# Kernel tuning notes

Measured on AMD Instinct MI355X. Metric: run time of the kernel, lower is better.

## Reference

```python
import jax, jax.numpy as jnp
import numpy as np

B = 131072            # number of supervoxel areas (vmapped)
H, W = 8, 16          # mask_new / mask_old shape
DX, DY = 16, 16       # diameter_x, diameter_y -> mask_combined / image shape
DIM_STRIDE = 0
TV = 2                # translation_val


def _grad(x, axis):
    # numpy-style gradient, unit spacing: central diff interior, one-sided edges
    x = jnp.moveaxis(x, axis, 0)
    g = jnp.concatenate([x[1:2] - x[0:1], (x[2:] - x[:-2]) * 0.5, x[-1:] - x[-2:-1]], axis=0)
    return jnp.moveaxis(g, 0, axis)


def get_diamond(diameter):
    r = diameter // 2
    def line(curr, idx):
        return jax.lax.dynamic_update_slice(curr, jnp.ones(diameter, jnp.float32), (jnp.abs(r - idx),))
    a = jax.vmap(line)(jnp.zeros((diameter, 2 * diameter), jnp.float32), jnp.arange(diameter)).astype(bool)
    b = jnp.flip(a)[:, diameter:]   # flip over both axes, keep right half
    a = a[:, :-diameter]
    return jnp.logical_and(a, b).astype(jnp.float32)


def translate(mask, axis, is_forward, tv, shape):
    lo = tv * (1 - is_forward)
    hi = shape[axis] - tv * is_forward
    m = jnp.take(mask, jnp.arange(lo, hi), axis=axis)
    pad = [[0, 0], [0, 0]]
    pad[axis][1 - is_forward] = tv
    return jnp.pad(m, pad)


def features(image, mask):
    mi = image * mask
    s = jnp.sum(mask)
    mean = jnp.sum(mi) / s
    var = jnp.sum(((mi - mean) * mask) ** 2) / s
    return jnp.stack([mean, var])


def single(image, mn, mo, diamond):
    # consistency loss
    p = jnp.pad(mo, ((1, 1), (1, 1)))
    g = _grad(p, DIM_STRIDE) ** 2
    g = g[1:-1, 1:-1]
    consistency = jnp.mean(jnp.maximum(mn - (g * 5.0 + mo * 5.0), 0.0))
    # intertwine 'f h w -> (h f) w'
    mc = jnp.stack([mn, mo], axis=1).reshape(DX, DY)
    rounding = jnp.mean(-((mc - (1.0 - mc)) ** 2))
    feats = jnp.stack([
        features(image, translate(mc, 0, 0, TV, (DX, DY))),
        features(image, translate(mc, 0, 1, TV, (DX, DY))),
        features(image, translate(mc, 1, 0, TV, (DX, DY))),
        features(image, translate(mc, 1, 1, TV, (DX, DY)))])
    fvar = jnp.mean(jnp.var(feats, axis=0))
    gi = _grad(image, DIM_STRIDE)
    gm = _grad(mc, DIM_STRIDE)
    edge = jnp.mean(0.5 * (gi - gm) ** 2 * gi)   # optax.l2_loss scaled by image gradient
    avg_cov = jnp.mean(0.5 * (mc - diamond) ** 2)
    mi = mc * image
    out_image = mc * (jnp.sum(mi) / jnp.sum(mc))
    return mc, out_image, consistency, rounding, fvar, edge, avg_cov


def setup_inputs() -> dict:
    key = jax.random.key(0)
    k1, k2, k3 = jax.random.split(key, 3)
    return {
        "resized_image": jax.random.normal(k1, (B, DX, DY), jnp.float32),
        "mask_new": jax.random.uniform(k2, (B, H, W), jnp.float32),
        "mask_old": jax.random.uniform(k3, (B, H, W), jnp.float32),
    }


def reference(resized_image, mask_new, mask_old):
    diamond = jnp.pad(get_diamond(DX - 1), ((0, 1), (0, 1)))  # (DX, DY)
    return jax.vmap(lambda im, mn, mo: single(im, mn, mo, diamond))(resized_image, mask_new, mask_old)
```

## Files before the change

kernel.cpp:

```cpp
#include <hip/hip_runtime.h>

template<int CTRL>
__device__ __forceinline__ float dppf(float v) {
    return __int_as_float(__builtin_amdgcn_update_dpp(
        0, __float_as_int(v), CTRL, 0xF, 0xF, true));
}

__device__ __forceinline__ float bfly16(float v) {
    v += dppf<0xB1>(v);
    v += dppf<0x4E>(v);
    v += dppf<0x141>(v);
    v += dppf<0x140>(v);
    return v;
}

__global__ __launch_bounds__(256) void apply_area_kernel(
    const float* __restrict__ img_g,
    const float* __restrict__ mn_g,
    const float* __restrict__ mo_g,
    float* __restrict__ out,
    int B)
{
    const int lane = threadIdx.x & 63;
    const int w    = threadIdx.x >> 6;
    const int q    = lane >> 4;
    const int c    = lane & 15;
    const int b    = blockIdx.x * 16 + w * 4 + q;
    if (b >= B) return;

    const float* imp = img_g + (size_t)b * 256 + c;
    const float* mnp = mn_g  + (size_t)b * 128 + c;
    const float* mop = mo_g  + (size_t)b * 128 + c;

    float im[16], mc[16];
#pragma unroll
    for (int r = 0; r < 16; ++r) im[r] = imp[r * 16];
#pragma unroll
    for (int i = 0; i < 8; ++i) {
        mc[2 * i]     = mnp[i * 16];
        mc[2 * i + 1] = mop[i * 16];
    }

    float c_acc = 0.f;
#pragma unroll
    for (int i = 0; i < 8; ++i) {
        float mo_i = mc[2 * i + 1];
        float mo_m = (i > 0) ? mc[2 * i - 1] : 0.f;
        float mo_p = (i < 7) ? mc[2 * i + 3] : 0.f;
        float g = 0.5f * (mo_p - mo_m);
        c_acc += fmaxf(mc[2 * i] - 5.f * (g * g + mo_i), 0.f);
    }

    float e_acc = 0.f, r_acc = 0.f, a_acc = 0.f, smi = 0.f, S1 = 0.f, S2 = 0.f;
#pragma unroll
    for (int r = 0; r < 16; ++r) {
        float gi = (r == 0)  ? im[1] - im[0]
                 : (r == 15) ? im[15] - im[14]
                 : 0.5f * (im[r + 1] - im[r - 1]);
        float gm = (r == 0)  ? mc[1] - mc[0]
                 : (r == 15) ? mc[15] - mc[14]
                 : 0.5f * (mc[r + 1] - mc[r - 1]);
        float d = gi - gm;
        e_acc += 0.5f * d * d * gi;
        float tw = 2.f * mc[r] - 1.f;
        r_acc += tw * tw;
        int abr = (r > 7) ? r - 7 : 7 - r;
        float dia = (r < 15 && c >= abr && c <= 14 - abr) ? 1.f : 0.f;
        float dd = mc[r] - dia;
        a_acc += 0.5f * dd * dd;
        S1 += mc[r];
        S2 += mc[r] * mc[r];
        smi += mc[r] * im[r];
    }

    float B0 = 0, D0 = 0, E0 = 0, B1 = 0, D1 = 0, E1 = 0;
    float B2 = 0, D2 = 0, E2 = 0, B3 = 0, D3 = 0, E3 = 0;
#pragma unroll
    for (int r = 0; r < 16; ++r) {
        float t0v = (r < 14) ? mc[r + 2] : 0.f;
        float t1v = (r >= 2) ? mc[r - 2] : 0.f;
        float t2v = dppf<0x102>(mc[r]);
        float t3v = dppf<0x112>(mc[r]);
#define ACC(t, Bx, Dx, Ex) { float mi_ = (t) * im[r]; float tt_ = (t) * (t); \
        Bx += mi_; Dx = fmaf(tt_, mi_, Dx); float tm_ = (t) * mi_; Ex = fmaf(tm_, tm_, Ex); }
        ACC(t0v, B0, D0, E0)
        ACC(t1v, B1, D1, E1)
        ACC(t2v, B2, D2, E2)
        ACC(t3v, B3, D3, E3)
#undef ACC
    }
    float A0 = S1 - mc[0] - mc[1];
    float C0 = S2 - mc[0] * mc[0] - mc[1] * mc[1];
    float A1 = S1 - mc[14] - mc[15];
    float C1 = S2 - mc[14] * mc[14] - mc[15] * mc[15];
    float A2 = dppf<0x102>(S1), C2 = dppf<0x102>(S2);
    float A3 = dppf<0x112>(S1), C3 = dppf<0x112>(S2);

    c_acc = bfly16(c_acc); r_acc = bfly16(r_acc);
    e_acc = bfly16(e_acc); a_acc = bfly16(a_acc);
    float smc = bfly16(S1); smi = bfly16(smi);
    A0 = bfly16(A0); A1 = bfly16(A1); A2 = bfly16(A2); A3 = bfly16(A3);
    B0 = bfly16(B0); B1 = bfly16(B1); B2 = bfly16(B2); B3 = bfly16(B3);
    C0 = bfly16(C0); C1 = bfly16(C1); C2 = bfly16(C2); C3 = bfly16(C3);
    D0 = bfly16(D0); D1 = bfly16(D1); D2 = bfly16(D2); D3 = bfly16(D3);
    E0 = bfly16(E0); E1 = bfly16(E1); E2 = bfly16(E2); E3 = bfly16(E3);

    const float scale = smi / smc;

    float* mco = out + (size_t)b * 256 + c;
    float* oio = out + (size_t)B * 256 + (size_t)b * 256 + c;
#pragma unroll
    for (int r = 0; r < 16; ++r) {
        mco[r * 16] = mc[r];
        oio[r * 16] = mc[r] * scale;
    }

    if (c == 0) {
        float m0 = B0 / A0, m1 = B1 / A1, m2 = B2 / A2, m3 = B3 / A3;
        float v0 = (E0 - 2.f * m0 * D0 + m0 * m0 * C0) / A0;
        float v1 = (E1 - 2.f * m1 * D1 + m1 * m1 * C1) / A1;
        float v2 = (E2 - 2.f * m2 * D2 + m2 * m2 * C2) / A2;
        float v3 = (E3 - 2.f * m3 * D3 + m3 * m3 * C3) / A3;

        float fm = 0.25f * (m0 + m1 + m2 + m3);
        float dm0 = m0 - fm, dm1 = m1 - fm, dm2 = m2 - fm, dm3 = m3 - fm;
        float vm = 0.25f * (dm0 * dm0 + dm1 * dm1 + dm2 * dm2 + dm3 * dm3);
        float fv = 0.25f * (v0 + v1 + v2 + v3);
        float dv0 = v0 - fv, dv1 = v1 - fv, dv2 = v2 - fv, dv3 = v3 - fv;
        float vv = 0.25f * (dv0 * dv0 + dv1 * dv1 + dv2 * dv2 + dv3 * dv3);

        float* s = out + (size_t)B * 512;
        s[b]                 = c_acc * (1.f / 128.f);
        s[(size_t)B + b]     = -r_acc * (1.f / 256.f);
        s[2 * (size_t)B + b] = 0.5f * (vm + vv);
        s[3 * (size_t)B + b] = e_acc * (1.f / 256.f);
        s[4 * (size_t)B + b] = a_acc * (1.f / 256.f);
    }
}

extern "C" void kernel_launch(void* const* d_in, const int* in_sizes, int n_in,
                              void* d_out, int out_size, void* d_ws, size_t ws_size,
                              hipStream_t stream) {
    const float* img = (const float*)d_in[0];
    const float* mn  = (const float*)d_in[1];
    const float* mo  = (const float*)d_in[2];
    float* out = (float*)d_out;
    const int B = in_sizes[0] / 256;
    const int blocks = (B + 15) / 16;
    apply_area_kernel<<<blocks, 256, 0, stream>>>(img, mn, mo, out, B);
}
```

Before: 105.2 us.

## Process two columns per lane with float2 accesses and nontemporal stores

Remaps each area onto 8 lanes, each handling two adjacent columns, so loads and stores use 64-bit vector accesses and cross-lane reductions shrink to 8-lane butterflies. Neighbor-column shifts now use row-shift-by-one DPP with boundary masks, since two areas share a DPP row. Output stores become nontemporal to avoid polluting caches. This halves thread count per area and raises per-thread register use.

```diff
diff --git a/kernel.cpp b/kernel.cpp
--- a/kernel.cpp
+++ b/kernel.cpp
@@ -1,4 +1,6 @@
 #include <hip/hip_runtime.h>
+
+typedef float vf2 __attribute__((ext_vector_type(2)));
 
 template<int CTRL>
 __device__ __forceinline__ float dppf(float v) {
@@ -6,11 +8,10 @@
         0, __float_as_int(v), CTRL, 0xF, 0xF, true));
 }
 
-__device__ __forceinline__ float bfly16(float v) {
+__device__ __forceinline__ float bfly8(float v) {
     v += dppf<0xB1>(v);
     v += dppf<0x4E>(v);
     v += dppf<0x141>(v);
-    v += dppf<0x140>(v);
     return v;
 }
 
@@ -23,99 +24,106 @@
 {
     const int lane = threadIdx.x & 63;
     const int w    = threadIdx.x >> 6;
-    const int q    = lane >> 4;
-    const int c    = lane & 15;
-    const int b    = blockIdx.x * 16 + w * 4 + q;
+    const int q    = lane >> 3;
+    const int l    = lane & 7;
+    const int b    = blockIdx.x * 32 + w * 8 + q;
     if (b >= B) return;
 
-    const float* imp = img_g + (size_t)b * 256 + c;
-    const float* mnp = mn_g  + (size_t)b * 128 + c;
-    const float* mop = mo_g  + (size_t)b * 128 + c;
+    const vf2* im2 = reinterpret_cast<const vf2*>(img_g) + (size_t)b * 128 + l;
+    const vf2* mn2 = reinterpret_cast<const vf2*>(mn_g)  + (size_t)b * 64  + l;
+    const vf2* mo2 = reinterpret_cast<const vf2*>(mo_g)  + (size_t)b * 64  + l;
 
-    float im[16], mc[16];
+    float imx[16], imy[16], mcx[16], mcy[16];
 #pragma unroll
-    for (int r = 0; r < 16; ++r) im[r] = imp[r * 16];
+    for (int r = 0; r < 16; ++r) { vf2 v = im2[r * 8]; imx[r] = v.x; imy[r] = v.y; }
 #pragma unroll
     for (int i = 0; i < 8; ++i) {
-        mc[2 * i]     = mnp[i * 16];
-        mc[2 * i + 1] = mop[i * 16];
+        vf2 a = mn2[i * 8]; mcx[2*i]   = a.x; mcy[2*i]   = a.y;
+        vf2 o = mo2[i * 8]; mcx[2*i+1] = o.x; mcy[2*i+1] = o.y;
     }
 
     float c_acc = 0.f;
 #pragma unroll
     for (int i = 0; i < 8; ++i) {
-        float mo_i = mc[2 * i + 1];
-        float mo_m = (i > 0) ? mc[2 * i - 1] : 0.f;
-        float mo_p = (i < 7) ? mc[2 * i + 3] : 0.f;
-        float g = 0.5f * (mo_p - mo_m);
-        c_acc += fmaxf(mc[2 * i] - 5.f * (g * g + mo_i), 0.f);
+        float mx_m = (i > 0) ? mcx[2*i-1] : 0.f, my_m = (i > 0) ? mcy[2*i-1] : 0.f;
+        float mx_p = (i < 7) ? mcx[2*i+3] : 0.f, my_p = (i < 7) ? mcy[2*i+3] : 0.f;
+        float gx = 0.5f * (mx_p - mx_m), gy = 0.5f * (my_p - my_m);
+        c_acc += fmaxf(mcx[2*i] - 5.f * (gx*gx + mcx[2*i+1]), 0.f);
+        c_acc += fmaxf(mcy[2*i] - 5.f * (gy*gy + mcy[2*i+1]), 0.f);
     }
 
     float e_acc = 0.f, r_acc = 0.f, a_acc = 0.f, smi = 0.f, S1 = 0.f, S2 = 0.f;
+    const int c0 = 2 * l, c1 = 2 * l + 1;
 #pragma unroll
     for (int r = 0; r < 16; ++r) {
-        float gi = (r == 0)  ? im[1] - im[0]
-                 : (r == 15) ? im[15] - im[14]
-                 : 0.5f * (im[r + 1] - im[r - 1]);
-        float gm = (r == 0)  ? mc[1] - mc[0]
-                 : (r == 15) ? mc[15] - mc[14]
-                 : 0.5f * (mc[r + 1] - mc[r - 1]);
-        float d = gi - gm;
-        e_acc += 0.5f * d * d * gi;
-        float tw = 2.f * mc[r] - 1.f;
-        r_acc += tw * tw;
         int abr = (r > 7) ? r - 7 : 7 - r;
-        float dia = (r < 15 && c >= abr && c <= 14 - abr) ? 1.f : 0.f;
-        float dd = mc[r] - dia;
-        a_acc += 0.5f * dd * dd;
-        S1 += mc[r];
-        S2 += mc[r] * mc[r];
-        smi += mc[r] * im[r];
+        bool drow = (r < 15);
+#define COMP(imA, mcA, cc) { \
+        float gi = (r == 0)  ? imA[1] - imA[0] \
+                 : (r == 15) ? imA[15] - imA[14] \
+                 : 0.5f * (imA[r + 1] - imA[r - 1]); \
+        float gm = (r == 0)  ? mcA[1] - mcA[0] \
+                 : (r == 15) ? mcA[15] - mcA[14] \
+                 : 0.5f * (mcA[r + 1] - mcA[r - 1]); \
+        float d = gi - gm; e_acc += 0.5f * d * d * gi; \
+        float tw = 2.f * mcA[r] - 1.f; r_acc += tw * tw; \
+        float dia = (drow && (cc) >= abr && (cc) <= 14 - abr) ? 1.f : 0.f; \
+        float dd = mcA[r] - dia; a_acc += 0.5f * dd * dd; \
+        S1 += mcA[r]; S2 += mcA[r] * mcA[r]; smi += mcA[r] * imA[r]; }
+        COMP(imx, mcx, c0)
+        COMP(imy, mcy, c1)
+#undef COMP
     }
 
-    float B0 = 0, D0 = 0, E0 = 0, B1 = 0, D1 = 0, E1 = 0;
-    float B2 = 0, D2 = 0, E2 = 0, B3 = 0, D3 = 0, E3 = 0;
+    const float mz7 = (l == 7) ? 0.f : 1.f;
+    const float mz0 = (l == 0) ? 0.f : 1.f;
+    float B0=0,D0=0,E0=0, B1=0,D1=0,E1=0, B2=0,D2=0,E2=0, B3=0,D3=0,E3=0;
 #pragma unroll
     for (int r = 0; r < 16; ++r) {
-        float t0v = (r < 14) ? mc[r + 2] : 0.f;
-        float t1v = (r >= 2) ? mc[r - 2] : 0.f;
-        float t2v = dppf<0x102>(mc[r]);
-        float t3v = dppf<0x112>(mc[r]);
-#define ACC(t, Bx, Dx, Ex) { float mi_ = (t) * im[r]; float tt_ = (t) * (t); \
-        Bx += mi_; Dx = fmaf(tt_, mi_, Dx); float tm_ = (t) * mi_; Ex = fmaf(tm_, tm_, Ex); }
-        ACC(t0v, B0, D0, E0)
-        ACC(t1v, B1, D1, E1)
-        ACC(t2v, B2, D2, E2)
-        ACC(t3v, B3, D3, E3)
-#undef ACC
+        float t0x = (r < 14) ? mcx[r+2] : 0.f, t0y = (r < 14) ? mcy[r+2] : 0.f;
+        float t1x = (r >= 2) ? mcx[r-2] : 0.f, t1y = (r >= 2) ? mcy[r-2] : 0.f;
+        float t2x = dppf<0x101>(mcx[r]) * mz7, t2y = dppf<0x101>(mcy[r]) * mz7;
+        float t3x = dppf<0x111>(mcx[r]) * mz0, t3y = dppf<0x111>(mcy[r]) * mz0;
+#define ACC2(tx, ty, Bx, Dx, Ex) { \
+        float mix_ = (tx) * imx[r], miy_ = (ty) * imy[r]; \
+        Bx += mix_ + miy_; \
+        Dx += (tx)*(tx)*mix_ + (ty)*(ty)*miy_; \
+        float ax_ = (tx)*mix_, ay_ = (ty)*miy_; \
+        Ex += ax_*ax_ + ay_*ay_; }
+        ACC2(t0x, t0y, B0, D0, E0)
+        ACC2(t1x, t1y, B1, D1, E1)
+        ACC2(t2x, t2y, B2, D2, E2)
+        ACC2(t3x, t3y, B3, D3, E3)
+#undef ACC2
     }
-    float A0 = S1 - mc[0] - mc[1];
-    float C0 = S2 - mc[0] * mc[0] - mc[1] * mc[1];
-    float A1 = S1 - mc[14] - mc[15];
-    float C1 = S2 - mc[14] * mc[14] - mc[15] * mc[15];
-    float A2 = dppf<0x102>(S1), C2 = dppf<0x102>(S2);
-    float A3 = dppf<0x112>(S1), C3 = dppf<0x112>(S2);
+    float A0 = S1 - (mcx[0] + mcy[0] + mcx[1] + mcy[1]);
+    float C0 = S2 - (mcx[0]*mcx[0] + mcy[0]*mcy[0] + mcx[1]*mcx[1] + mcy[1]*mcy[1]);
+    float A1 = S1 - (mcx[14] + mcy[14] + mcx[15] + mcy[15]);
+    float C1 = S2 - (mcx[14]*mcx[14] + mcy[14]*mcy[14] + mcx[15]*mcx[15] + mcy[15]*mcy[15]);
+    float A2 = dppf<0x101>(S1) * mz7, C2 = dppf<0x101>(S2) * mz7;
+    float A3 = dppf<0x111>(S1) * mz0, C3 = dppf<0x111>(S2) * mz0;
 
-    c_acc = bfly16(c_acc); r_acc = bfly16(r_acc);
-    e_acc = bfly16(e_acc); a_acc = bfly16(a_acc);
-    float smc = bfly16(S1); smi = bfly16(smi);
-    A0 = bfly16(A0); A1 = bfly16(A1); A2 = bfly16(A2); A3 = bfly16(A3);
-    B0 = bfly16(B0); B1 = bfly16(B1); B2 = bfly16(B2); B3 = bfly16(B3);
-    C0 = bfly16(C0); C1 = bfly16(C1); C2 = bfly16(C2); C3 = bfly16(C3);
-    D0 = bfly16(D0); D1 = bfly16(D1); D2 = bfly16(D2); D3 = bfly16(D3);
-    E0 = bfly16(E0); E1 = bfly16(E1); E2 = bfly16(E2); E3 = bfly16(E3);
+    c_acc = bfly8(c_acc); r_acc = bfly8(r_acc);
+    e_acc = bfly8(e_acc); a_acc = bfly8(a_acc);
+    float smc = bfly8(S1); smi = bfly8(smi);
+    A0 = bfly8(A0); A1 = bfly8(A1); A2 = bfly8(A2); A3 = bfly8(A3);
+    B0 = bfly8(B0); B1 = bfly8(B1); B2 = bfly8(B2); B3 = bfly8(B3);
+    C0 = bfly8(C0); C1 = bfly8(C1); C2 = bfly8(C2); C3 = bfly8(C3);
+    D0 = bfly8(D0); D1 = bfly8(D1); D2 = bfly8(D2); D3 = bfly8(D3);
+    E0 = bfly8(E0); E1 = bfly8(E1); E2 = bfly8(E2); E3 = bfly8(E3);
 
     const float scale = smi / smc;
-
-    float* mco = out + (size_t)b * 256 + c;
-    float* oio = out + (size_t)B * 256 + (size_t)b * 256 + c;
+    vf2* mco = reinterpret_cast<vf2*>(out) + (size_t)b * 128 + l;
+    vf2* oio = reinterpret_cast<vf2*>(out) + (size_t)B * 128 + (size_t)b * 128 + l;
 #pragma unroll
     for (int r = 0; r < 16; ++r) {
-        mco[r * 16] = mc[r];
-        oio[r * 16] = mc[r] * scale;
+        vf2 mv; mv.x = mcx[r]; mv.y = mcy[r];
+        vf2 ov; ov.x = mcx[r] * scale; ov.y = mcy[r] * scale;
+        __builtin_nontemporal_store(mv, mco + r * 8);
+        __builtin_nontemporal_store(ov, oio + r * 8);
     }
 
-    if (c == 0) {
+    if (l == 0) {
         float m0 = B0 / A0, m1 = B1 / A1, m2 = B2 / A2, m3 = B3 / A3;
         float v0 = (E0 - 2.f * m0 * D0 + m0 * m0 * C0) / A0;
         float v1 = (E1 - 2.f * m1 * D1 + m1 * m1 * C1) / A1;
@@ -124,17 +132,17 @@
 
         float fm = 0.25f * (m0 + m1 + m2 + m3);
         float dm0 = m0 - fm, dm1 = m1 - fm, dm2 = m2 - fm, dm3 = m3 - fm;
-        float vm = 0.25f * (dm0 * dm0 + dm1 * dm1 + dm2 * dm2 + dm3 * dm3);
+        float vm = 0.25f * (dm0*dm0 + dm1*dm1 + dm2*dm2 + dm3*dm3);
         float fv = 0.25f * (v0 + v1 + v2 + v3);
         float dv0 = v0 - fv, dv1 = v1 - fv, dv2 = v2 - fv, dv3 = v3 - fv;
-        float vv = 0.25f * (dv0 * dv0 + dv1 * dv1 + dv2 * dv2 + dv3 * dv3);
+        float vv = 0.25f * (dv0*dv0 + dv1*dv1 + dv2*dv2 + dv3*dv3);
 
         float* s = out + (size_t)B * 512;
-        s[b]                 = c_acc * (1.f / 128.f);
-        s[(size_t)B + b]     = -r_acc * (1.f / 256.f);
-        s[2 * (size_t)B + b] = 0.5f * (vm + vv);
-        s[3 * (size_t)B + b] = e_acc * (1.f / 256.f);
-        s[4 * (size_t)B + b] = a_acc * (1.f / 256.f);
+        __builtin_nontemporal_store(c_acc * (1.f / 128.f), s + b);
+        __builtin_nontemporal_store(-r_acc * (1.f / 256.f), s + (size_t)B + b);
+        __builtin_nontemporal_store(0.5f * (vm + vv), s + 2*(size_t)B + b);
+        __builtin_nontemporal_store(e_acc * (1.f / 256.f), s + 3*(size_t)B + b);
+        __builtin_nontemporal_store(a_acc * (1.f / 256.f), s + 4*(size_t)B + b);
     }
 }
 
@@ -146,6 +154,6 @@
     const float* mo  = (const float*)d_in[2];
     float* out = (float*)d_out;
     const int B = in_sizes[0] / 256;
-    const int blocks = (B + 15) / 16;
+    const int blocks = (B + 31) / 32;
     apply_area_kernel<<<blocks, 256, 0, stream>>>(img, mn, mo, out, B);
 }
```

Measured after the change: 103.1 us. -2.1%, faster.

## Remap to 4 lanes per area with float4 loads, nontemporal stores

Applied to the files above, without the earlier changes.

Each area is now handled by 4 lanes instead of 16, and each lane owns 4 adjacent columns loaded as float4 vectors. This cuts the cross-lane reduction to two DPP steps and makes global loads and stores 128-bit wide. Output stores become nontemporal, and the scalar outputs are spread across lanes instead of all coming from one lane. Each thread now holds about four times as many values in registers, and a launch-bounds occupancy hint is added to cap that register use.

```diff
diff --git a/kernel.cpp b/kernel.cpp
--- a/kernel.cpp
+++ b/kernel.cpp
@@ -1,4 +1,6 @@
 #include <hip/hip_runtime.h>
+
+typedef float vf4 __attribute__((ext_vector_type(4)));
 
 template<int CTRL>
 __device__ __forceinline__ float dppf(float v) {
@@ -6,15 +8,15 @@
         0, __float_as_int(v), CTRL, 0xF, 0xF, true));
 }
 
-__device__ __forceinline__ float bfly16(float v) {
+__device__ __forceinline__ float bfly4(float v) {
     v += dppf<0xB1>(v);
     v += dppf<0x4E>(v);
-    v += dppf<0x141>(v);
-    v += dppf<0x140>(v);
     return v;
 }
 
-__global__ __launch_bounds__(256) void apply_area_kernel(
+__device__ __forceinline__ float hsum4(vf4 v) { return (v.x + v.y) + (v.z + v.w); }
+
+__global__ __launch_bounds__(256, 2) void apply_area_kernel(
     const float* __restrict__ img_g,
     const float* __restrict__ mn_g,
     const float* __restrict__ mo_g,
@@ -23,119 +25,140 @@
 {
     const int lane = threadIdx.x & 63;
     const int w    = threadIdx.x >> 6;
-    const int q    = lane >> 4;
-    const int c    = lane & 15;
-    const int b    = blockIdx.x * 16 + w * 4 + q;
+    const int q    = lane >> 2;
+    const int l4   = lane & 3;
+    const int b    = blockIdx.x * 64 + w * 16 + q;
     if (b >= B) return;
 
-    const float* imp = img_g + (size_t)b * 256 + c;
-    const float* mnp = mn_g  + (size_t)b * 128 + c;
-    const float* mop = mo_g  + (size_t)b * 128 + c;
+    const vf4* im4 = reinterpret_cast<const vf4*>(img_g) + (size_t)b * 64 + l4;
+    const vf4* mn4 = reinterpret_cast<const vf4*>(mn_g)  + (size_t)b * 32 + l4;
+    const vf4* mo4 = reinterpret_cast<const vf4*>(mo_g)  + (size_t)b * 32 + l4;
 
-    float im[16], mc[16];
+    vf4 im[16], mc[16];
 #pragma unroll
-    for (int r = 0; r < 16; ++r) im[r] = imp[r * 16];
+    for (int r = 0; r < 16; ++r) im[r] = im4[r * 4];
 #pragma unroll
     for (int i = 0; i < 8; ++i) {
-        mc[2 * i]     = mnp[i * 16];
-        mc[2 * i + 1] = mop[i * 16];
+        mc[2 * i]     = mn4[i * 4];
+        mc[2 * i + 1] = mo4[i * 4];
+    }
+    asm volatile("" ::: "memory");
+
+    const vf4 z4 = {0.f, 0.f, 0.f, 0.f};
+
+    vf4 cv = z4;
+#pragma unroll
+    for (int i = 0; i < 8; ++i) {
+        vf4 mm = (i > 0) ? mc[2 * i - 1] : z4;
+        vf4 mp = (i < 7) ? mc[2 * i + 3] : z4;
+        vf4 g = 0.5f * (mp - mm);
+        vf4 t = mc[2 * i] - 5.f * (g * g + mc[2 * i + 1]);
+        cv.x += fmaxf(t.x, 0.f); cv.y += fmaxf(t.y, 0.f);
+        cv.z += fmaxf(t.z, 0.f); cv.w += fmaxf(t.w, 0.f);
     }
 
-    float c_acc = 0.f;
+    vf4 ev = z4, rv = z4, av = z4, smiv = z4, S1v = z4, S2v = z4;
+    const int cb = 4 * l4;
 #pragma unroll
-    for (int i = 0; i < 8; ++i) {
-        float mo_i = mc[2 * i + 1];
-        float mo_m = (i > 0) ? mc[2 * i - 1] : 0.f;
-        float mo_p = (i < 7) ? mc[2 * i + 3] : 0.f;
-        float g = 0.5f * (mo_p - mo_m);
-        c_acc += fmaxf(mc[2 * i] - 5.f * (g * g + mo_i), 0.f);
+    for (int r = 0; r < 16; ++r) {
+        vf4 gi = (r == 0)  ? im[1] - im[0]
+               : (r == 15) ? im[15] - im[14]
+               : 0.5f * (im[r + 1] - im[r - 1]);
+        vf4 gm = (r == 0)  ? mc[1] - mc[0]
+               : (r == 15) ? mc[15] - mc[14]
+               : 0.5f * (mc[r + 1] - mc[r - 1]);
+        vf4 d = gi - gm;
+        ev += 0.5f * d * d * gi;
+        vf4 tw = 2.f * mc[r] - 1.f;
+        rv += tw * tw;
+        int abr = (r > 7) ? r - 7 : 7 - r;
+        int hi = 14 - abr;
+        vf4 dia;
+        dia.x = (r < 15 && cb + 0 >= abr && cb + 0 <= hi) ? 1.f : 0.f;
+        dia.y = (r < 15 && cb + 1 >= abr && cb + 1 <= hi) ? 1.f : 0.f;
+        dia.z = (r < 15 && cb + 2 >= abr && cb + 2 <= hi) ? 1.f : 0.f;
+        dia.w = (r < 15 && cb + 3 >= abr && cb + 3 <= hi) ? 1.f : 0.f;
+        vf4 dd = mc[r] - dia;
+        av += 0.5f * dd * dd;
+        S1v += mc[r];
+        S2v += mc[r] * mc[r];
+        smiv += mc[r] * im[r];
     }
 
-    float e_acc = 0.f, r_acc = 0.f, a_acc = 0.f, smi = 0.f, S1 = 0.f, S2 = 0.f;
+    const float mz3 = (l4 == 3) ? 0.f : 1.f;
+    const float mz0 = (l4 == 0) ? 0.f : 1.f;
+    vf4 B0v = z4, D0v = z4, E0v = z4, B1v = z4, D1v = z4, E1v = z4;
+    vf4 B2v = z4, D2v = z4, E2v = z4, B3v = z4, D3v = z4, E3v = z4;
 #pragma unroll
     for (int r = 0; r < 16; ++r) {
-        float gi = (r == 0)  ? im[1] - im[0]
-                 : (r == 15) ? im[15] - im[14]
-                 : 0.5f * (im[r + 1] - im[r - 1]);
-        float gm = (r == 0)  ? mc[1] - mc[0]
-                 : (r == 15) ? mc[15] - mc[14]
-                 : 0.5f * (mc[r + 1] - mc[r - 1]);
-        float d = gi - gm;
-        e_acc += 0.5f * d * d * gi;
-        float tw = 2.f * mc[r] - 1.f;
-        r_acc += tw * tw;
-        int abr = (r > 7) ? r - 7 : 7 - r;
-        float dia = (r < 15 && c >= abr && c <= 14 - abr) ? 1.f : 0.f;
-        float dd = mc[r] - dia;
-        a_acc += 0.5f * dd * dd;
-        S1 += mc[r];
-        S2 += mc[r] * mc[r];
-        smi += mc[r] * im[r];
+        vf4 t0 = (r < 14) ? mc[r + 2] : z4;
+        vf4 t1 = (r >= 2) ? mc[r - 2] : z4;
+        vf4 m = mc[r];
+        vf4 t2, t3;
+        t2.x = m.z; t2.y = m.w;
+        t2.z = dppf<0x101>(m.x) * mz3; t2.w = dppf<0x101>(m.y) * mz3;
+        t3.x = dppf<0x111>(m.z) * mz0; t3.y = dppf<0x111>(m.w) * mz0;
+        t3.z = m.x; t3.w = m.y;
+#define ACC4(t, Bx, Dx, Ex) { vf4 mi_ = (t) * im[r]; Bx += mi_; \
+        Dx += (t) * (t) * mi_; vf4 a_ = (t) * mi_; Ex += a_ * a_; }
+        ACC4(t0, B0v, D0v, E0v)
+        ACC4(t1, B1v, D1v, E1v)
+        ACC4(t2, B2v, D2v, E2v)
+        ACC4(t3, B3v, D3v, E3v)
+#undef ACC4
     }
 
-    float B0 = 0, D0 = 0, E0 = 0, B1 = 0, D1 = 0, E1 = 0;
-    float B2 = 0, D2 = 0, E2 = 0, B3 = 0, D3 = 0, E3 = 0;
+    float S1 = hsum4(S1v), S2 = hsum4(S2v);
+    float A0 = S1 - hsum4(mc[0]) - hsum4(mc[1]);
+    float C0 = S2 - hsum4(mc[0] * mc[0]) - hsum4(mc[1] * mc[1]);
+    float A1 = S1 - hsum4(mc[14]) - hsum4(mc[15]);
+    float C1 = S2 - hsum4(mc[14] * mc[14]) - hsum4(mc[15] * mc[15]);
+    float A2 = S1v.z + S1v.w + (dppf<0x101>(S1v.x) + dppf<0x101>(S1v.y)) * mz3;
+    float C2 = S2v.z + S2v.w + (dppf<0x101>(S2v.x) + dppf<0x101>(S2v.y)) * mz3;
+    float A3 = S1v.x + S1v.y + (dppf<0x111>(S1v.z) + dppf<0x111>(S1v.w)) * mz0;
+    float C3 = S2v.x + S2v.y + (dppf<0x111>(S2v.z) + dppf<0x111>(S2v.w)) * mz0;
+
+    float c_s = bfly4(hsum4(cv)), r_s = bfly4(hsum4(rv));
+    float e_s = bfly4(hsum4(ev)), a_s = bfly4(hsum4(av));
+    float smc = bfly4(S1),        smi = bfly4(hsum4(smiv));
+    A0 = bfly4(A0); A1 = bfly4(A1); A2 = bfly4(A2); A3 = bfly4(A3);
+    C0 = bfly4(C0); C1 = bfly4(C1); C2 = bfly4(C2); C3 = bfly4(C3);
+    float B0 = bfly4(hsum4(B0v)), B1 = bfly4(hsum4(B1v));
+    float B2 = bfly4(hsum4(B2v)), B3 = bfly4(hsum4(B3v));
+    float D0 = bfly4(hsum4(D0v)), D1 = bfly4(hsum4(D1v));
+    float D2 = bfly4(hsum4(D2v)), D3 = bfly4(hsum4(D3v));
+    float E0 = bfly4(hsum4(E0v)), E1 = bfly4(hsum4(E1v));
+    float E2 = bfly4(hsum4(E2v)), E3 = bfly4(hsum4(E3v));
+
+    const float scale = smi / smc;
+    vf4* mco = reinterpret_cast<vf4*>(out) + (size_t)b * 64 + l4;
+    vf4* oio = reinterpret_cast<vf4*>(out) + (size_t)B * 64 + (size_t)b * 64 + l4;
 #pragma unroll
     for (int r = 0; r < 16; ++r) {
-        float t0v = (r < 14) ? mc[r + 2] : 0.f;
-        float t1v = (r >= 2) ? mc[r - 2] : 0.f;
-        float t2v = dppf<0x102>(mc[r]);
-        float t3v = dppf<0x112>(mc[r]);
-#define ACC(t, Bx, Dx, Ex) { float mi_ = (t) * im[r]; float tt_ = (t) * (t); \
-        Bx += mi_; Dx = fmaf(tt_, mi_, Dx); float tm_ = (t) * mi_; Ex = fmaf(tm_, tm_, Ex); }
-        ACC(t0v, B0, D0, E0)
-        ACC(t1v, B1, D1, E1)
-        ACC(t2v, B2, D2, E2)
-        ACC(t3v, B3, D3, E3)
-#undef ACC
-    }
-    float A0 = S1 - mc[0] - mc[1];
-    float C0 = S2 - mc[0] * mc[0] - mc[1] * mc[1];
-    float A1 = S1 - mc[14] - mc[15];
-    float C1 = S2 - mc[14] * mc[14] - mc[15] * mc[15];
-    float A2 = dppf<0x102>(S1), C2 = dppf<0x102>(S2);
-    float A3 = dppf<0x112>(S1), C3 = dppf<0x112>(S2);
-
-    c_acc = bfly16(c_acc); r_acc = bfly16(r_acc);
-    e_acc = bfly16(e_acc); a_acc = bfly16(a_acc);
-    float smc = bfly16(S1); smi = bfly16(smi);
-    A0 = bfly16(A0); A1 = bfly16(A1); A2 = bfly16(A2); A3 = bfly16(A3);
-    B0 = bfly16(B0); B1 = bfly16(B1); B2 = bfly16(B2); B3 = bfly16(B3);
-    C0 = bfly16(C0); C1 = bfly16(C1); C2 = bfly16(C2); C3 = bfly16(C3);
-    D0 = bfly16(D0); D1 = bfly16(D1); D2 = bfly16(D2); D3 = bfly16(D3);
-    E0 = bfly16(E0); E1 = bfly16(E1); E2 = bfly16(E2); E3 = bfly16(E3);
-
-    const float scale = smi / smc;
-
-    float* mco = out + (size_t)b * 256 + c;
-    float* oio = out + (size_t)B * 256 + (size_t)b * 256 + c;
-#pragma unroll
-    for (int r = 0; r < 16; ++r) {
-        mco[r * 16] = mc[r];
-        oio[r * 16] = mc[r] * scale;
+        __builtin_nontemporal_store(mc[r], mco + r * 4);
+        __builtin_nontemporal_store(mc[r] * scale, oio + r * 4);
     }
 
-    if (c == 0) {
-        float m0 = B0 / A0, m1 = B1 / A1, m2 = B2 / A2, m3 = B3 / A3;
-        float v0 = (E0 - 2.f * m0 * D0 + m0 * m0 * C0) / A0;
-        float v1 = (E1 - 2.f * m1 * D1 + m1 * m1 * C1) / A1;
-        float v2 = (E2 - 2.f * m2 * D2 + m2 * m2 * C2) / A2;
-        float v3 = (E3 - 2.f * m3 * D3 + m3 * m3 * C3) / A3;
+    float m0 = B0 / A0, m1 = B1 / A1, m2 = B2 / A2, m3 = B3 / A3;
+    float v0 = (E0 - 2.f * m0 * D0 + m0 * m0 * C0) / A0;
+    float v1 = (E1 - 2.f * m1 * D1 + m1 * m1 * C1) / A1;
+    float v2 = (E2 - 2.f * m2 * D2 + m2 * m2 * C2) / A2;
+    float v3 = (E3 - 2.f * m3 * D3 + m3 * m3 * C3) / A3;
+    float fm = 0.25f * (m0 + m1 + m2 + m3);
+    float dm0 = m0 - fm, dm1 = m1 - fm, dm2 = m2 - fm, dm3 = m3 - fm;
+    float vm = 0.25f * (dm0 * dm0 + dm1 * dm1 + dm2 * dm2 + dm3 * dm3);
+    float fv = 0.25f * (v0 + v1 + v2 + v3);
+    float dv0 = v0 - fv, dv1 = v1 - fv, dv2 = v2 - fv, dv3 = v3 - fv;
+    float vv = 0.25f * (dv0 * dv0 + dv1 * dv1 + dv2 * dv2 + dv3 * dv3);
 
-        float fm = 0.25f * (m0 + m1 + m2 + m3);
-        float dm0 = m0 - fm, dm1 = m1 - fm, dm2 = m2 - fm, dm3 = m3 - fm;
-        float vm = 0.25f * (dm0 * dm0 + dm1 * dm1 + dm2 * dm2 + dm3 * dm3);
-        float fv = 0.25f * (v0 + v1 + v2 + v3);
-        float dv0 = v0 - fv, dv1 = v1 - fv, dv2 = v2 - fv, dv3 = v3 - fv;
-        float vv = 0.25f * (dv0 * dv0 + dv1 * dv1 + dv2 * dv2 + dv3 * dv3);
-
-        float* s = out + (size_t)B * 512;
-        s[b]                 = c_acc * (1.f / 128.f);
-        s[(size_t)B + b]     = -r_acc * (1.f / 256.f);
-        s[2 * (size_t)B + b] = 0.5f * (vm + vv);
-        s[3 * (size_t)B + b] = e_acc * (1.f / 256.f);
-        s[4 * (size_t)B + b] = a_acc * (1.f / 256.f);
-    }
+    float sv = (l4 == 0) ? c_s * (1.f / 128.f)
+             : (l4 == 1) ? -r_s * (1.f / 256.f)
+             : (l4 == 2) ? 0.5f * (vm + vv)
+             :             e_s * (1.f / 256.f);
+    float* s = out + (size_t)B * 512;
+    __builtin_nontemporal_store(sv, s + (size_t)l4 * B + b);
+    if (l4 == 0)
+        __builtin_nontemporal_store(a_s * (1.f / 256.f), s + 4 * (size_t)B + b);
 }
 
 extern "C" void kernel_launch(void* const* d_in, const int* in_sizes, int n_in,
@@ -146,6 +169,6 @@
     const float* mo  = (const float*)d_in[2];
     float* out = (float*)d_out;
     const int B = in_sizes[0] / 256;
-    const int blocks = (B + 15) / 16;
+    const int blocks = (B + 63) / 64;
     apply_area_kernel<<<blocks, 256, 0, stream>>>(img, mn, mo, out, B);
 }
```

Result: no change. 106.7 us (+1.4%).
